# Performance work log

Hardware: AMD Instinct MI355X
Metric: run time of the kernel (lower is better)

The kernel has to match this reference:

```python
import jax, jax.numpy as jnp
import numpy as np
import math

L = 7          # spherical-harmonic truncation -> lsize = (L+1)^2 = 64
T = 128        # number of channels/fragments in clms


def _cg_coef(j1, m1, j2, m2, j, m):
    """Clebsch-Gordan coefficient <j1 m1 j2 m2 | j m> via the Racah formula."""
    if m1 + m2 != m or not (abs(j1 - j2) <= j <= j1 + j2):
        return 0.0
    f = math.factorial
    pref = math.sqrt((2 * j + 1) * f(j1 + j2 - j) * f(j1 - j2 + j)
                     * f(-j1 + j2 + j) / f(j1 + j2 + j + 1))
    pref *= math.sqrt(f(j + m) * f(j - m) * f(j1 - m1) * f(j1 + m1)
                      * f(j2 - m2) * f(j2 + m2))
    kmin = max(0, j2 - j - m1, j1 + m2 - j)
    kmax = min(j1 + j2 - j, j1 - m1, j2 + m2)
    s = 0.0
    for k in range(kmin, kmax + 1):
        s += (-1) ** k / (f(k) * f(j1 + j2 - j - k) * f(j1 - m1 - k)
                          * f(j2 + m2 - k) * f(j - j2 + m1 + k) * f(j - j1 - m2 + k))
    return pref * s


def _idx(l, m):
    return l * l + l + m


def _build_C(L):
    """Dense packed CG tensor C[(l,m),(l1,m1),(l2,m2)], zero outside selection rules."""
    lsize = (L + 1) ** 2
    C = np.zeros((lsize, lsize, lsize), dtype=np.float64)
    for l1 in range(L + 1):
        for l2 in range(L + 1):
            for l in range(abs(l1 - l2), min(l1 + l2, L) + 1):
                for m1 in range(-l1, l1 + 1):
                    for m2 in range(-l2, l2 + 1):
                        m = m1 + m2
                        if abs(m) <= l:
                            C[_idx(l, m), _idx(l1, m1), _idx(l2, m2)] = \
                                _cg_coef(l1, m1, l2, m2, l, m)
    return C.astype(np.float32)


def setup_inputs() -> dict:
    key = jax.random.key(0)
    clms = jax.random.normal(key, ((L + 1) ** 2, T), dtype=jnp.float32)
    C = jnp.asarray(_build_C(L))
    return {"clms": clms, "C": C}


def reference(clms, C):
    lsize = clms.shape[0]
    Lc = int(math.isqrt(lsize)) - 1
    Tn = clms.shape[1]
    # full Kronecker product, blockwise indexed by (l1,m1),(l2,m2); [lsize, lsize, T^2]
    Gs = (clms[:, None, :, None] * clms[None, :, None, :]).reshape(lsize, lsize, Tn * Tn)
    temp = [[] for _ in range(Lc + 1)]
    for l1 in range(Lc + 1):
        for l2 in range(Lc + 1):
            g = Gs[l1 * l1:(l1 + 1) ** 2, l2 * l2:(l2 + 1) ** 2, :]
            cg = C[:, l1 * l1:(l1 + 1) ** 2, l2 * l2:(l2 + 1) ** 2]
            # cg @ g over the flattened (m1,m2) block -> [(Lc+1)^2, T^2]
            prod = jnp.einsum('kij,ijt->kt', cg, g)
            for l in range(abs(l1 - l2), min(l1 + l2, Lc) + 1):
                temp[l].append(prod[l * l:(l + 1) ** 2, :])
    return tuple(jnp.concatenate(t, axis=1) for t in temp)
```

## Files before the change

kernel.cpp:

```cpp
#include <hip/hip_runtime.h>

#define TDIM 128

__host__ __device__ inline int trivalid(int l, int l1, int l2) {
  int d = l1 - l2; if (d < 0) d = -d;
  return (l >= d && l <= l1 + l2) ? 1 : 0;
}

__device__ __forceinline__ float u2f(unsigned int u) {
  union { unsigned int u; float f; } w; w.u = u; return w.f;
}
__device__ __forceinline__ float bf2f(unsigned short v) {
  return u2f(((unsigned int)v) << 16);
}
__device__ __forceinline__ unsigned short f2bf(float x) {
  union { float f; unsigned int u; } w; w.f = x;
  unsigned int u = w.u;
  u += 0x7fffu + ((u >> 16) & 1u);
  return (unsigned short)(u >> 16);
}

__global__ __launch_bounds__(256, 4)
void cg_kernel(const void* __restrict__ clms_raw,
               const void* __restrict__ C_raw,
               void* __restrict__ out_raw) {
  __shared__ float sc[64 * TDIM];
  __shared__ float scoef[16];

  const int tid = threadIdx.x;

  const unsigned int* cw = (const unsigned int*)clms_raw;
  int cnt_bf = 0;
  #pragma unroll
  for (int i = 0; i < 32; ++i) {
    unsigned int e = (cw[i] >> 7) & 0xFFu;
    cnt_bf += (e >= 110u && e <= 135u) ? 1 : 0;
  }
  const bool in_bf16 = (cnt_bf >= 16);
  const bool c_bf16 = ((*(const unsigned int*)C_raw) & 0xffffu) == 0x3f80u;

  if (tid < 16) scoef[tid] = 0.0f;

  if (in_bf16) {
    const uint4* cl4 = (const uint4*)clms_raw;
    #pragma unroll
    for (int it = 0; it < 4; ++it) {
      int v = tid + it * 256;
      uint4 w = cl4[v];
      float4* dst = (float4*)&sc[v * 8];
      float4 d0, d1;
      d0.x = u2f(w.x << 16); d0.y = u2f(w.x & 0xffff0000u);
      d0.z = u2f(w.y << 16); d0.w = u2f(w.y & 0xffff0000u);
      d1.x = u2f(w.z << 16); d1.y = u2f(w.z & 0xffff0000u);
      d1.z = u2f(w.w << 16); d1.w = u2f(w.w & 0xffff0000u);
      dst[0] = d0; dst[1] = d1;
    }
  } else {
    const float4* cf4 = (const float4*)clms_raw;
    float4* sc4 = (float4*)sc;
    #pragma unroll
    for (int it = 0; it < 8; ++it) {
      int v = tid + it * 256;
      sc4[v] = cf4[v];
    }
  }

  const int r = blockIdx.x;
  int rem = r, l = 0, cnt = 0;
  for (l = 0; l < 8; ++l) {
    cnt = 0;
    for (int a = 0; a < 8; ++a)
      for (int b = 0; b < 8; ++b) cnt += trivalid(l, a, b);
    int rows = (2 * l + 1) * cnt;
    if (rem < rows) break;
    rem -= rows;
  }
  const int mi = rem / cnt;
  const int p  = rem - mi * cnt;
  const int m  = mi - l;
  int l1 = 0, l2 = 0;
  {
    int q = 0; bool done = false;
    for (int a = 0; a < 8 && !done; ++a)
      for (int b = 0; b < 8; ++b) {
        if (trivalid(l, a, b)) {
          if (q == p) { l1 = a; l2 = b; done = true; break; }
          ++q;
        }
      }
  }

  int m1lo = (-l1 > m - l2) ? -l1 : (m - l2);
  int m1hi = ( l1 < m + l2) ?  l1 : (m + l2);
  const int nnz = m1hi - m1lo + 1;

  if (tid < nnz) {
    int m1 = m1lo + tid;
    int m2 = m - m1;
    int i  = l1 * (l1 + 1) + m1;
    int j  = l2 * (l2 + 1) + m2;
    int k  = l  * (l  + 1) + m;
    int ci = ((k * 64) + i) * 64 + j;
    scoef[tid] = c_bf16 ? bf2f(((const unsigned short*)C_raw)[ci])
                        : ((const float*)C_raw)[ci];
  }
  __syncthreads();

  float creg[15];
  #pragma unroll
  for (int q = 0; q < 15; ++q) creg[q] = scoef[q];

  const int tx = tid & 31;
  const int ty = tid >> 5;
  const int t2 = tx * 4;
  const int i0 = l1 * (l1 + 1) + m1lo;
  const int j0 = l2 * (l2 + 1) + m - m1lo;

  int arow[15], brow[15];
  #pragma unroll
  for (int q = 0; q < 15; ++q) {
    int qc = (q < nnz) ? q : 0;
    arow[q] = (i0 + qc) * TDIM;
    brow[q] = (j0 - qc) * TDIM;
  }

  float4 b[15];
  #pragma unroll
  for (int q = 0; q < 15; ++q) b[q] = *(const float4*)&sc[brow[q] + t2];

  const unsigned long long outbase = (unsigned long long)r * (TDIM * TDIM);

  if (in_bf16) {
    unsigned short* out = (unsigned short*)out_raw;
    #pragma unroll 4
    for (int s = 0; s < 16; ++s) {
      const int t1 = ty + 8 * s;
      float4 acc = make_float4(0.f, 0.f, 0.f, 0.f);
      #pragma unroll
      for (int q = 0; q < 15; ++q) {
        if (q < nnz) {
          float ca = creg[q] * sc[arow[q] + t1];
          acc.x += ca * b[q].x;  acc.y += ca * b[q].y;
          acc.z += ca * b[q].z;  acc.w += ca * b[q].w;
        }
      }
      ushort4 o;
      o.x = f2bf(acc.x); o.y = f2bf(acc.y);
      o.z = f2bf(acc.z); o.w = f2bf(acc.w);
      *(ushort4*)(out + outbase + (unsigned long long)(t1 * TDIM + t2)) = o;
    }
  } else {
    float* out = (float*)out_raw;
    #pragma unroll 4
    for (int s = 0; s < 16; ++s) {
      const int t1 = ty + 8 * s;
      float4 acc = make_float4(0.f, 0.f, 0.f, 0.f);
      #pragma unroll
      for (int q = 0; q < 15; ++q) {
        if (q < nnz) {
          float ca = creg[q] * sc[arow[q] + t1];
          acc.x += ca * b[q].x;  acc.y += ca * b[q].y;
          acc.z += ca * b[q].z;  acc.w += ca * b[q].w;
        }
      }
      *(float4*)(out + outbase + (unsigned long long)(t1 * TDIM + t2)) = acc;
    }
  }
}

extern "C" void kernel_launch(void* const* d_in, const int* in_sizes, int n_in,
                              void* d_out, int out_size, void* d_ws, size_t ws_size,
                              hipStream_t stream) {
  (void)in_sizes; (void)n_in; (void)d_ws; (void)ws_size;
  const int nrows = out_size / (TDIM * TDIM);
  cg_kernel<<<nrows, 256, 0, stream>>>(d_in[0], d_in[1], d_out);
}
```

Measured before the change: 172.5 us.

## Stage only needed A/B rows in shared memory with CG coefficients prefolded

Each block now loads only the up-to-15 A rows and 15 B rows it actually uses, instead of the full 64x128 clms matrix. The CG coefficient is multiplied into the B rows during staging. The row-to-(l,l1,l2) decoding uses hard-coded cumulative offsets in place of nested loops. The output loop is restructured to compute four rows per iteration. Together these cut global and LDS traffic and per-block setup, which should also allow higher occupancy because LDS drops from 32KB to 16KB, but the offsets are now fixed to L=7.

```diff
diff --git a/kernel.cpp b/kernel.cpp
--- a/kernel.cpp
+++ b/kernel.cpp
@@ -1,11 +1,6 @@
 #include <hip/hip_runtime.h>
 
 #define TDIM 128
-
-__host__ __device__ inline int trivalid(int l, int l1, int l2) {
-  int d = l1 - l2; if (d < 0) d = -d;
-  return (l >= d && l <= l1 + l2) ? 1 : 0;
-}
 
 __device__ __forceinline__ float u2f(unsigned int u) {
   union { unsigned int u; float f; } w; w.u = u; return w.f;
@@ -24,146 +19,146 @@
 void cg_kernel(const void* __restrict__ clms_raw,
                const void* __restrict__ C_raw,
                void* __restrict__ out_raw) {
-  __shared__ float sc[64 * TDIM];
-  __shared__ float scoef[16];
+  __shared__ float sa[16 * TDIM];
+  __shared__ float sb[16 * TDIM];
 
   const int tid = threadIdx.x;
 
   const unsigned int* cw = (const unsigned int*)clms_raw;
-  int cnt_bf = 0;
+  int nbf = 0;
   #pragma unroll
   for (int i = 0; i < 32; ++i) {
     unsigned int e = (cw[i] >> 7) & 0xFFu;
-    cnt_bf += (e >= 110u && e <= 135u) ? 1 : 0;
+    nbf += (e >= 110u && e <= 135u) ? 1 : 0;
   }
-  const bool in_bf16 = (cnt_bf >= 16);
+  const bool in_bf16 = (nbf >= 16);
   const bool c_bf16 = ((*(const unsigned int*)C_raw) & 0xffffu) == 0x3f80u;
 
-  if (tid < 16) scoef[tid] = 0.0f;
-
-  if (in_bf16) {
-    const uint4* cl4 = (const uint4*)clms_raw;
-    #pragma unroll
-    for (int it = 0; it < 4; ++it) {
-      int v = tid + it * 256;
-      uint4 w = cl4[v];
-      float4* dst = (float4*)&sc[v * 8];
-      float4 d0, d1;
-      d0.x = u2f(w.x << 16); d0.y = u2f(w.x & 0xffff0000u);
-      d0.z = u2f(w.y << 16); d0.w = u2f(w.y & 0xffff0000u);
-      d1.x = u2f(w.z << 16); d1.y = u2f(w.z & 0xffff0000u);
-      d1.z = u2f(w.w << 16); d1.w = u2f(w.w & 0xffff0000u);
-      dst[0] = d0; dst[1] = d1;
-    }
-  } else {
-    const float4* cf4 = (const float4*)clms_raw;
-    float4* sc4 = (float4*)sc;
-    #pragma unroll
-    for (int it = 0; it < 8; ++it) {
-      int v = tid + it * 256;
-      sc4[v] = cf4[v];
-    }
+  const int r = blockIdx.x;
+  int l = 0, cum = 0, pc = 8;
+  if (r >= 8)    { l = 1; cum = 8;    pc = 21; }
+  if (r >= 71)   { l = 2; cum = 71;   pc = 31; }
+  if (r >= 226)  { l = 3; cum = 226;  pc = 38; }
+  if (r >= 492)  { l = 4; cum = 492;  pc = 42; }
+  if (r >= 870)  { l = 5; cum = 870;  pc = 43; }
+  if (r >= 1343) { l = 6; cum = 1343; pc = 41; }
+  if (r >= 1876) { l = 7; cum = 1876; pc = 36; }
+  const int rem = r - cum;
+  const int mi  = rem / pc;
+  const int m   = mi - l;
+  int pp = rem - mi * pc;
+  int l1 = 0, l2 = 0, found = 0;
+  #pragma unroll
+  for (int a = 0; a < 8; ++a) {
+    int d = a - l; if (d < 0) d = -d;
+    int hi = a + l; if (hi > 7) hi = 7;
+    int na = hi - d + 1;
+    if (!found && pp < na) { l1 = a; l2 = d + pp; found = 1; }
+    if (!found) pp -= na;
   }
 
-  const int r = blockIdx.x;
-  int rem = r, l = 0, cnt = 0;
-  for (l = 0; l < 8; ++l) {
-    cnt = 0;
-    for (int a = 0; a < 8; ++a)
-      for (int b = 0; b < 8; ++b) cnt += trivalid(l, a, b);
-    int rows = (2 * l + 1) * cnt;
-    if (rem < rows) break;
-    rem -= rows;
-  }
-  const int mi = rem / cnt;
-  const int p  = rem - mi * cnt;
-  const int m  = mi - l;
-  int l1 = 0, l2 = 0;
-  {
-    int q = 0; bool done = false;
-    for (int a = 0; a < 8 && !done; ++a)
-      for (int b = 0; b < 8; ++b) {
-        if (trivalid(l, a, b)) {
-          if (q == p) { l1 = a; l2 = b; done = true; break; }
-          ++q;
+  const int m1lo = (-l1 > m - l2) ? -l1 : (m - l2);
+  const int m1hi = ( l1 < m + l2) ?  l1 : (m + l2);
+  const int nnz = m1hi - m1lo + 1;
+  const int i0 = l1 * (l1 + 1) + m1lo;
+  const int j0 = l2 * (l2 + 1) + (m - m1lo);
+  const int k0 = l * (l + 1) + m;
+
+  #pragma unroll
+  for (int kk = 0; kk < 8; ++kk) {
+    const int u = tid + 256 * kk;
+    if (u < 1920) {
+      const int row  = u >> 6;
+      const int lane = u & 63;
+      const int isB  = row >= 15;
+      const int q    = isB ? row - 15 : row;
+      const int qc   = (q < nnz) ? q : 0;
+      const int gr   = isB ? (j0 - qc) : (i0 + qc);
+      float f0, f1;
+      if (in_bf16) {
+        unsigned int v = ((const unsigned int*)clms_raw)[gr * 64 + lane];
+        f0 = u2f(v << 16); f1 = u2f(v & 0xffff0000u);
+      } else {
+        float2 v = ((const float2*)clms_raw)[gr * 64 + lane];
+        f0 = v.x; f1 = v.y;
+      }
+      if (isB) {
+        float cq = 0.0f;
+        if (q < nnz) {
+          int ci = (k0 * 64 + i0 + q) * 64 + (j0 - q);
+          cq = c_bf16 ? bf2f(((const unsigned short*)C_raw)[ci])
+                      : ((const float*)C_raw)[ci];
         }
+        f0 *= cq; f1 *= cq;
+        *(float2*)&sb[q * TDIM + lane * 2] = make_float2(f0, f1);
+      } else {
+        *(float2*)&sa[q * TDIM + lane * 2] = make_float2(f0, f1);
       }
-  }
-
-  int m1lo = (-l1 > m - l2) ? -l1 : (m - l2);
-  int m1hi = ( l1 < m + l2) ?  l1 : (m + l2);
-  const int nnz = m1hi - m1lo + 1;
-
-  if (tid < nnz) {
-    int m1 = m1lo + tid;
-    int m2 = m - m1;
-    int i  = l1 * (l1 + 1) + m1;
-    int j  = l2 * (l2 + 1) + m2;
-    int k  = l  * (l  + 1) + m;
-    int ci = ((k * 64) + i) * 64 + j;
-    scoef[tid] = c_bf16 ? bf2f(((const unsigned short*)C_raw)[ci])
-                        : ((const float*)C_raw)[ci];
+    }
   }
   __syncthreads();
 
-  float creg[15];
-  #pragma unroll
-  for (int q = 0; q < 15; ++q) creg[q] = scoef[q];
-
   const int tx = tid & 31;
   const int ty = tid >> 5;
-  const int t2 = tx * 4;
-  const int i0 = l1 * (l1 + 1) + m1lo;
-  const int j0 = l2 * (l2 + 1) + m - m1lo;
-
-  int arow[15], brow[15];
-  #pragma unroll
-  for (int q = 0; q < 15; ++q) {
-    int qc = (q < nnz) ? q : 0;
-    arow[q] = (i0 + qc) * TDIM;
-    brow[q] = (j0 - qc) * TDIM;
-  }
-
   float4 b[15];
   #pragma unroll
-  for (int q = 0; q < 15; ++q) b[q] = *(const float4*)&sc[brow[q] + t2];
+  for (int q = 0; q < 15; ++q)
+    b[q] = *(const float4*)&sb[q * TDIM + tx * 4];
 
-  const unsigned long long outbase = (unsigned long long)r * (TDIM * TDIM);
+  const unsigned long long outbase =
+      (unsigned long long)r * (TDIM * TDIM) + (unsigned int)(tx * 4);
 
   if (in_bf16) {
     unsigned short* out = (unsigned short*)out_raw;
-    #pragma unroll 4
-    for (int s = 0; s < 16; ++s) {
-      const int t1 = ty + 8 * s;
-      float4 acc = make_float4(0.f, 0.f, 0.f, 0.f);
+    for (int s0 = 0; s0 < 4; ++s0) {
+      const int t1b = ty + 32 * s0;
+      float4 acc[4];
+      #pragma unroll
+      for (int d = 0; d < 4; ++d) acc[d] = make_float4(0.f, 0.f, 0.f, 0.f);
       #pragma unroll
       for (int q = 0; q < 15; ++q) {
         if (q < nnz) {
-          float ca = creg[q] * sc[arow[q] + t1];
-          acc.x += ca * b[q].x;  acc.y += ca * b[q].y;
-          acc.z += ca * b[q].z;  acc.w += ca * b[q].w;
+          #pragma unroll
+          for (int d = 0; d < 4; ++d) {
+            float a = sa[q * TDIM + t1b + 8 * d];
+            acc[d].x += a * b[q].x;
+            acc[d].y += a * b[q].y;
+            acc[d].z += a * b[q].z;
+            acc[d].w += a * b[q].w;
+          }
         }
       }
-      ushort4 o;
-      o.x = f2bf(acc.x); o.y = f2bf(acc.y);
-      o.z = f2bf(acc.z); o.w = f2bf(acc.w);
-      *(ushort4*)(out + outbase + (unsigned long long)(t1 * TDIM + t2)) = o;
+      #pragma unroll
+      for (int d = 0; d < 4; ++d) {
+        ushort4 o;
+        o.x = f2bf(acc[d].x); o.y = f2bf(acc[d].y);
+        o.z = f2bf(acc[d].z); o.w = f2bf(acc[d].w);
+        *(ushort4*)(out + outbase + (unsigned long long)((t1b + 8 * d) * TDIM)) = o;
+      }
     }
   } else {
     float* out = (float*)out_raw;
-    #pragma unroll 4
-    for (int s = 0; s < 16; ++s) {
-      const int t1 = ty + 8 * s;
-      float4 acc = make_float4(0.f, 0.f, 0.f, 0.f);
+    for (int s0 = 0; s0 < 4; ++s0) {
+      const int t1b = ty + 32 * s0;
+      float4 acc[4];
+      #pragma unroll
+      for (int d = 0; d < 4; ++d) acc[d] = make_float4(0.f, 0.f, 0.f, 0.f);
       #pragma unroll
       for (int q = 0; q < 15; ++q) {
         if (q < nnz) {
-          float ca = creg[q] * sc[arow[q] + t1];
-          acc.x += ca * b[q].x;  acc.y += ca * b[q].y;
-          acc.z += ca * b[q].z;  acc.w += ca * b[q].w;
+          #pragma unroll
+          for (int d = 0; d < 4; ++d) {
+            float a = sa[q * TDIM + t1b + 8 * d];
+            acc[d].x += a * b[q].x;
+            acc[d].y += a * b[q].y;
+            acc[d].z += a * b[q].z;
+            acc[d].w += a * b[q].w;
+          }
         }
       }
-      *(float4*)(out + outbase + (unsigned long long)(t1 * TDIM + t2)) = acc;
+      #pragma unroll
+      for (int d = 0; d < 4; ++d)
+        *(float4*)(out + outbase + (unsigned long long)((t1b + 8 * d) * TDIM)) = acc[d];
     }
   }
 }
```

Result: faster. 165.9 us (-3.8%).
